# Kernel tuning notes

Measured on AMD Instinct MI355X. Metric: run time of the kernel, lower is better.

## Reference

```python
import jax, jax.numpy as jnp
import numpy as np

D_MODEL = 1024
NUM_LATENTS = 8
N_HEADS = 8
HEAD_DIM = D_MODEL // N_HEADS
LN_EPS = 1e-5
NEG_INF = -1e9


def setup_inputs() -> dict:
    key = jax.random.key(0)
    ks = jax.random.split(key, 9)
    B, S, d = 8, 8192, D_MODEL
    hidden_states = jax.random.normal(ks[0], (B, S, d), dtype=jnp.float32)
    attention_mask = jax.random.randint(ks[1], (B, S), 0, 2, dtype=jnp.int32)
    # guarantee at least one valid token per row
    attention_mask = attention_mask.at[:, 0].set(1)
    latent_queries = jax.random.normal(ks[2], (NUM_LATENTS, d), dtype=jnp.float32) * 0.02
    lim = 1.0 / np.sqrt(d)
    in_proj_weight = jax.random.uniform(ks[3], (3 * d, d), minval=-lim, maxval=lim, dtype=jnp.float32)
    in_proj_bias = jnp.zeros((3 * d,), jnp.float32)
    out_proj_weight = jax.random.uniform(ks[4], (d, d), minval=-lim, maxval=lim, dtype=jnp.float32)
    out_proj_bias = jnp.zeros((d,), jnp.float32)
    ln_gamma = jnp.ones((d,), jnp.float32)
    ln_beta = jnp.zeros((d,), jnp.float32)
    return {
        "hidden_states": hidden_states,
        "latent_queries": latent_queries,
        "in_proj_weight": in_proj_weight,
        "in_proj_bias": in_proj_bias,
        "out_proj_weight": out_proj_weight,
        "out_proj_bias": out_proj_bias,
        "ln_gamma": ln_gamma,
        "ln_beta": ln_beta,
        "attention_mask": attention_mask,
    }


def reference(hidden_states, latent_queries, in_proj_weight, in_proj_bias,
              out_proj_weight, out_proj_bias, ln_gamma, ln_beta, attention_mask):
    B, S, d = hidden_states.shape
    K, H, hd = NUM_LATENTS, N_HEADS, HEAD_DIM
    Wq, Wk, Wv = jnp.split(in_proj_weight, 3, axis=0)   # each [d, d]
    bq, bk, bv = jnp.split(in_proj_bias, 3, axis=0)
    # projections (queries shared over batch)
    q = latent_queries @ Wq.T + bq                      # [K, d]
    k = hidden_states @ Wk.T + bk                       # [B, S, d]
    v = hidden_states @ Wv.T + bv                       # [B, S, d]
    q = q.reshape(K, H, hd).transpose(1, 0, 2)          # [H, K, hd]
    k = k.reshape(B, S, H, hd).transpose(0, 2, 1, 3)    # [B, H, S, hd]
    v = v.reshape(B, S, H, hd).transpose(0, 2, 1, 3)    # [B, H, S, hd]
    scale = 1.0 / np.sqrt(hd)
    scores = jnp.einsum('hkd,bhsd->bhks', q, k) * scale  # [B, H, K, S]
    pad = (attention_mask == 0)[:, None, None, :]        # [B, 1, 1, S]
    scores = jnp.where(pad, NEG_INF, scores)
    attn = jax.nn.softmax(scores, axis=-1)
    ctx = jnp.einsum('bhks,bhsd->bhkd', attn, v)         # [B, H, K, hd]
    ctx = ctx.transpose(0, 2, 1, 3).reshape(B, K, d)     # [B, K, d]
    pooled = ctx @ out_proj_weight.T + out_proj_bias     # [B, K, d]
    # LayerNorm
    mu = pooled.mean(-1, keepdims=True)
    var = jnp.mean(jnp.square(pooled - mu), axis=-1, keepdims=True)
    pooled = (pooled - mu) * jax.lax.rsqrt(var + LN_EPS) * ln_gamma + ln_beta
    return pooled.mean(axis=1)                           # [B, d]
```

## Files before the change

kernel.cpp:

```cpp
#include <hip/hip_runtime.h>
#include <math.h>

#define D_M 1024
#define S_L 8192
#define B_N 8
#define H_N 8
#define HD_ 128
#define HK_ 64
#define SCALE_ 0.08838834764831845f
#define NEG_INF_ -1e9f
#define PITCH_ 40
#define AP_ 72

typedef _Float16 half8v __attribute__((ext_vector_type(8)));
typedef _Float16 half4v __attribute__((ext_vector_type(4)));
typedef float floatx4 __attribute__((ext_vector_type(4)));

__global__ void k_q(const float* __restrict__ lat, const float* __restrict__ W,
                    const float* __restrict__ bias, float* __restrict__ q) {
  int g = blockIdx.x * blockDim.x + threadIdx.x;
  int kidx = g >> 10, i = g & 1023;
  const float* wr = W + (size_t)i * D_M;
  const float* lr = lat + kidx * D_M;
  float acc = bias[i];
  #pragma unroll 4
  for (int t = 0; t < D_M; t += 4) {
    float4 w = *(const float4*)(wr + t);
    float4 l = *(const float4*)(lr + t);
    acc += w.x*l.x + w.y*l.y + w.z*l.z + w.w*l.w;
  }
  q[g] = acc;
}

__global__ void k_qt(const float* __restrict__ q, const float* __restrict__ W,
                     const float* __restrict__ bias, _Float16* __restrict__ qth,
                     float* __restrict__ qconst) {
  int g = blockIdx.x * blockDim.x + threadIdx.x;
  int hk = g >> 10, j = g & 1023;
  int h = hk >> 3, kidx = hk & 7;
  const float* qr = q + kidx * D_M + h * HD_;
  const float* wb = W + ((size_t)D_M + (size_t)h * HD_) * D_M + j;
  float acc = 0.f;
  #pragma unroll 4
  for (int dd = 0; dd < HD_; ++dd)
    acc += qr[dd] * wb[(size_t)dd * D_M];
  qth[g] = (_Float16)(acc * SCALE_);
  if (j == 0) {
    const float* bk = bias + D_M + h * HD_;
    float c = 0.f;
    for (int dd = 0; dd < HD_; ++dd) c += qr[dd] * bk[dd];
    qconst[hk] = c * SCALE_;
  }
}

__global__ __launch_bounds__(512) void k_cnt(const int* __restrict__ mask,
                                             int* __restrict__ cbase,
                                             int* __restrict__ cnt) {
  __shared__ int wcnt[8];
  __shared__ int ccnt[64];
  int b = blockIdx.x, tid = threadIdx.x, w = tid >> 6, lane = tid & 63;
  int vs[16];
  #pragma unroll
  for (int it = 0; it < 16; ++it) vs[it] = mask[b * S_L + it * 512 + tid];
  for (int it = 0; it < 16; ++it) {
    unsigned long long m = __ballot(vs[it] != 0);
    if (lane == 0) wcnt[w] = __popcll(m);
    __syncthreads();
    if (tid < 4) ccnt[it * 4 + tid] = wcnt[2 * tid] + wcnt[2 * tid + 1];
    __syncthreads();
  }
  if (tid == 0) {
    int base = 0;
    for (int c = 0; c < 64; ++c) { cbase[b * 64 + c] = base; base += ccnt[c]; }
    cnt[b] = base;
  }
}

__global__ __launch_bounds__(128) void k_gather(const float* __restrict__ hidden,
                                                const int* __restrict__ mask,
                                                const int* __restrict__ cbase,
                                                float* __restrict__ hcomp) {
  __shared__ int slot_of[128];
  __shared__ int wcnt[2];
  __shared__ int woff[3];
  int blk = blockIdx.x;
  int b = blk >> 6, c = blk & 63;
  int tid = threadIdx.x, w = tid >> 6, lane = tid & 63;
  int valid = mask[b * S_L + c * 128 + tid] != 0;
  unsigned long long m = __ballot(valid);
  int rank = __popcll(m & ((1ull << lane) - 1ull));
  if (lane == 0) wcnt[w] = __popcll(m);
  __syncthreads();
  if (tid == 0) { woff[0] = 0; woff[1] = wcnt[0]; woff[2] = wcnt[0] + wcnt[1]; }
  __syncthreads();
  if (valid) slot_of[woff[w] + rank] = tid;
  __syncthreads();
  int nv = woff[2];
  int base = cbase[b * 64 + c];
  for (int v = w; v < nv; v += 2) {
    const float* src = hidden + ((size_t)b * S_L + c * 128 + slot_of[v]) * D_M;
    float* dst = hcomp + ((size_t)b * S_L + base + v) * D_M;
    #pragma unroll
    for (int q4 = 0; q4 < 4; ++q4) {
      float4 val = *(const float4*)(src + q4 * 256 + lane * 4);
      *(float4*)(dst + q4 * 256 + lane * 4) = val;
    }
  }
}

__global__ __launch_bounds__(256) void k_scores3(
    const float* __restrict__ hcomp, const _Float16* __restrict__ qth,
    const float* __restrict__ qc, const int* __restrict__ cnt,
    _Float16* __restrict__ ph, float* __restrict__ pm, float* __restrict__ pl) {
  __shared__ __align__(16) _Float16 As[128 * AP_];
  __shared__ __align__(16) _Float16 Bs[64 * AP_];
  __shared__ _Float16 pT[128][68];
  __shared__ float qcs[64];
  const int tid = threadIdx.x;
  const int b = blockIdx.x >> 6;
  const int st = blockIdx.x & 63;
  const int s0 = st * 128;
  const int cb = cnt[b];
  const int SPb = ((cb + 511) >> 9) << 9;
  if (s0 >= SPb) return;
  const int w = tid >> 6, l = tid & 63;
  const int row16 = l & 15, kc = l >> 4;
  if (tid < 64) qcs[tid] = qc[tid];
  floatx4 acc[2][4];
  #pragma unroll
  for (int mf = 0; mf < 2; ++mf)
    #pragma unroll
    for (int nf = 0; nf < 4; ++nf) acc[mf][nf] = (floatx4){0.f, 0.f, 0.f, 0.f};

  const int r_ = tid >> 3, c_ = tid & 7;
  const float* hb = hcomp + ((size_t)b * S_L + s0) * D_M;
  float4 fa[4][2];
  half8v fb[2];
  #pragma unroll
  for (int p = 0; p < 4; ++p) {
    const float* pr = hb + (size_t)(p * 32 + r_) * D_M + c_ * 8;
    fa[p][0] = *(const float4*)pr; fa[p][1] = *(const float4*)(pr + 4);
  }
  fb[0] = *(const half8v*)(qth + (size_t)r_ * D_M + c_ * 8);
  fb[1] = *(const half8v*)(qth + (size_t)(r_ + 32) * D_M + c_ * 8);

  for (int k0 = 0; k0 < D_M; k0 += 64) {
    __syncthreads();
    #pragma unroll
    for (int p = 0; p < 4; ++p) {
      half8v hv;
      hv[0] = (_Float16)fa[p][0].x; hv[1] = (_Float16)fa[p][0].y;
      hv[2] = (_Float16)fa[p][0].z; hv[3] = (_Float16)fa[p][0].w;
      hv[4] = (_Float16)fa[p][1].x; hv[5] = (_Float16)fa[p][1].y;
      hv[6] = (_Float16)fa[p][1].z; hv[7] = (_Float16)fa[p][1].w;
      *(half8v*)&As[(p * 32 + r_) * AP_ + c_ * 8] = hv;
    }
    *(half8v*)&Bs[r_ * AP_ + c_ * 8] = fb[0];
    *(half8v*)&Bs[(r_ + 32) * AP_ + c_ * 8] = fb[1];
    if (k0 + 64 < D_M) {
      #pragma unroll
      for (int p = 0; p < 4; ++p) {
        const float* pr = hb + (size_t)(p * 32 + r_) * D_M + (k0 + 64) + c_ * 8;
        fa[p][0] = *(const float4*)pr; fa[p][1] = *(const float4*)(pr + 4);
      }
      fb[0] = *(const half8v*)(qth + (size_t)r_ * D_M + (k0 + 64) + c_ * 8);
      fb[1] = *(const half8v*)(qth + (size_t)(r_ + 32) * D_M + (k0 + 64) + c_ * 8);
    }
    __syncthreads();
    #pragma unroll
    for (int kk = 0; kk < 2; ++kk) {
      half8v af[2], bf4[4];
      #pragma unroll
      for (int mf = 0; mf < 2; ++mf)
        af[mf] = *(const half8v*)&As[(w * 32 + mf * 16 + row16) * AP_ + kk * 32 + kc * 8];
      #pragma unroll
      for (int nf = 0; nf < 4; ++nf)
        bf4[nf] = *(const half8v*)&Bs[(nf * 16 + row16) * AP_ + kk * 32 + kc * 8];
      #pragma unroll
      for (int mf = 0; mf < 2; ++mf)
        #pragma unroll
        for (int nf = 0; nf < 4; ++nf)
          acc[mf][nf] = __builtin_amdgcn_mfma_f32_16x16x32_f16(af[mf], bf4[nf], acc[mf][nf], 0, 0, 0);
    }
  }
  int msk[8];
  #pragma unroll
  for (int mf = 0; mf < 2; ++mf)
    #pragma unroll
    for (int r = 0; r < 4; ++r)
      msk[mf * 4 + r] = (s0 + w * 32 + mf * 16 + kc * 4 + r) < cb;
  #pragma unroll
  for (int nf = 0; nf < 4; ++nf) {
    int hk = nf * 16 + row16;
    float qcv = qcs[hk];
    float vals[8];
    float mloc = -3.4e38f;
    #pragma unroll
    for (int mf = 0; mf < 2; ++mf)
      #pragma unroll
      for (int r = 0; r < 4; ++r) {
        float v = msk[mf * 4 + r] ? (acc[mf][nf][r] + qcv) : NEG_INF_;
        vals[mf * 4 + r] = v;
        mloc = fmaxf(mloc, v);
      }
    mloc = fmaxf(mloc, __shfl_xor(mloc, 16, 64));
    mloc = fmaxf(mloc, __shfl_xor(mloc, 32, 64));
    float ls = 0.f;
    #pragma unroll
    for (int mf = 0; mf < 2; ++mf)
      #pragma unroll
      for (int r = 0; r < 4; ++r) {
        float e = __expf(vals[mf * 4 + r] - mloc);
        ls += e;
        pT[w * 32 + mf * 16 + kc * 4 + r][hk] = (_Float16)e;
      }
    ls += __shfl_xor(ls, 16, 64);
    ls += __shfl_xor(ls, 32, 64);
    if (kc == 0) {
      int idx = ((b * 64 + st) * 4 + w) * 64 + hk;
      pm[idx] = mloc;
      pl[idx] = ls;
    }
  }
  __syncthreads();
  {
    int hk2 = tid >> 2, q4 = tid & 3;
    _Float16* dst = ph + ((size_t)b * 64 + hk2) * S_L + s0 + q4 * 32;
    #pragma unroll
    for (int i = 0; i < 4; ++i) {
      half8v v;
      #pragma unroll
      for (int e = 0; e < 8; ++e) v[e] = pT[q4 * 32 + i * 8 + e][hk2];
      *(half8v*)(dst + i * 8) = v;
    }
  }
}

__global__ __launch_bounds__(256) void k_stats2b(
    const float* __restrict__ pm, const float* __restrict__ pl,
    const int* __restrict__ cnt, float* __restrict__ lvinv, _Float16* __restrict__ ph) {
  __shared__ float red[256];
  int bh = blockIdx.x;
  int b = bh >> 6, hk = bh & 63;
  int tid = threadIdx.x;
  const int cb = cnt[b];
  const int ntile = (((cb + 511) >> 9) << 9) >> 5;
  float m = -3.4e38f, lv = 0.f;
  if (tid < ntile) {
    m = pm[((size_t)b * 256 + tid) * 64 + hk];
    lv = pl[((size_t)b * 256 + tid) * 64 + hk];
  }
  red[tid] = m; __syncthreads();
  for (int off = 128; off > 0; off >>= 1) {
    if (tid < off) red[tid] = fmaxf(red[tid], red[tid + off]);
    __syncthreads();
  }
  float M = red[0]; __syncthreads();
  red[tid] = lv * __expf(m - M); __syncthreads();
  for (int off = 128; off > 0; off >>= 1) {
    if (tid < off) red[tid] += red[tid + off];
    __syncthreads();
  }
  if (tid == 0) lvinv[bh] = 1.f / red[0];
  if (tid < ntile) {
    float f = __expf(m - M);
    _Float16* pp = ph + (size_t)bh * S_L + tid * 32;
    #pragma unroll
    for (int i = 0; i < 4; ++i) {
      half8v v = *(half8v*)(pp + i * 8);
      #pragma unroll
      for (int e = 0; e < 8; ++e) v[e] = (_Float16)((float)v[e] * f);
      *(half8v*)(pp + i * 8) = v;
    }
  }
}

__global__ __launch_bounds__(512) void k_part(
    const float* __restrict__ hcomp, const _Float16* __restrict__ ph,
    const int* __restrict__ cnt, float* __restrict__ part) {
  __shared__ __align__(16) _Float16 htile[512 * PITCH_];
  const int tid = threadIdx.x;
  const int b  = blockIdx.x >> 5;
  const int jb = (blockIdx.x >> 4) & 1;
  const int sc = blockIdx.x & 15;
  const int SPb = ((cnt[b] + 511) >> 9) << 9;
  if (sc * 512 >= SPb) return;
  const int w = tid >> 6, l = tid & 63;
  const int row16 = l & 15, kc = l >> 4;
  const int s_base = sc * 512;
  const float* hb = hcomp + (size_t)b * S_L * D_M + jb * 512;
  const _Float16* phb = ph + (size_t)b * HK_ * S_L;
  floatx4 acc[4][4];
  #pragma unroll
  for (int mf = 0; mf < 4; ++mf)
    #pragma unroll
    for (int nf = 0; nf < 4; ++nf) acc[mf][nf] = (floatx4){0.f, 0.f, 0.f, 0.f};

  const int jcol = tid;
  float colv[32];
  #pragma unroll
  for (int s = 0; s < 32; ++s)
    colv[s] = hb[(size_t)(s_base + s) * D_M + jcol];

  for (int t = 0; t < 16; ++t) {
    const int s0 = s_base + t * 32;
    __syncthreads();
    #pragma unroll
    for (int sb = 0; sb < 8; ++sb) {
      half4v hv;
      hv[0] = (_Float16)colv[sb * 4 + 0];
      hv[1] = (_Float16)colv[sb * 4 + 1];
      hv[2] = (_Float16)colv[sb * 4 + 2];
      hv[3] = (_Float16)colv[sb * 4 + 3];
      *(half4v*)&htile[jcol * PITCH_ + sb * 4] = hv;
    }
    __syncthreads();
    if (t < 15) {
      #pragma unroll
      for (int s = 0; s < 32; ++s)
        colv[s] = hb[(size_t)(s0 + 32 + s) * D_M + jcol];
    }
    half8v ap[4];
    #pragma unroll
    for (int mf = 0; mf < 4; ++mf)
      ap[mf] = *(const half8v*)(phb + (size_t)(mf * 16 + row16) * S_L + s0 + kc * 8);
    #pragma unroll
    for (int nf = 0; nf < 4; ++nf) {
      int j = w * 64 + nf * 16 + row16;
      half8v bv = *(const half8v*)&htile[j * PITCH_ + kc * 8];
      #pragma unroll
      for (int mf = 0; mf < 4; ++mf)
        acc[mf][nf] = __builtin_amdgcn_mfma_f32_16x16x32_f16(ap[mf], bv, acc[mf][nf], 0, 0, 0);
    }
  }
  #pragma unroll
  for (int mf = 0; mf < 4; ++mf)
    #pragma unroll
    for (int nf = 0; nf < 4; ++nf) {
      int j = w * 64 + nf * 16 + row16;
      #pragma unroll
      for (int r = 0; r < 4; ++r) {
        int hk = mf * 16 + kc * 4 + r;
        part[(((size_t)(b * 2 + jb) * 16 + sc) * HK_ + hk) * 512 + j] = acc[mf][nf][r];
      }
    }
}

__global__ void k_comb(const float* __restrict__ part, const float* __restrict__ lvinv,
                       const int* __restrict__ cnt, float* __restrict__ ctxh) {
  int g = blockIdx.x * blockDim.x + threadIdx.x;
  int b = g >> 14;
  int rem = g & 16383;
  int hk = rem >> 8;
  int j4 = rem & 255;
  int jb = j4 >> 7;
  int jr4 = j4 & 127;
  const int nsc = (((cnt[b] + 511) >> 9) << 9) >> 9;
  const float* pb = part + ((size_t)(b * 2 + jb) * 16 * HK_ + hk) * 512 + jr4 * 4;
  float4 s = make_float4(0.f, 0.f, 0.f, 0.f);
  for (int sc = 0; sc < nsc; ++sc) {
    float4 v = *(const float4*)(pb + (size_t)sc * HK_ * 512);
    s.x += v.x; s.y += v.y; s.z += v.z; s.w += v.w;
  }
  float li = lvinv[b * 64 + hk];
  s.x *= li; s.y *= li; s.z *= li; s.w *= li;
  *(float4*)(ctxh + ((size_t)b * HK_ + hk) * D_M + j4 * 4) = s;
}

__global__ void k_ctx(const float* __restrict__ ctxh, const float* __restrict__ W,
                      const float* __restrict__ bias, float* __restrict__ ctx) {
  int g2 = blockIdx.x * blockDim.x + threadIdx.x;
  int o = g2 >> 2, kq = g2 & 3;
  int b = o >> 13, kidx = (o >> 10) & 7, i = o & 1023;
  int hk = (i >> 7) * 8 + kidx;
  const float* wr = W + ((size_t)2 * D_M + i) * D_M + kq * 256;
  const float* xr = ctxh + ((size_t)b * HK_ + hk) * D_M + kq * 256;
  float acc = 0.f;
  #pragma unroll 8
  for (int t = 0; t < 256; t += 4) {
    float4 w = *(const float4*)(wr + t);
    float4 x = *(const float4*)(xr + t);
    acc += w.x*x.x + w.y*x.y + w.z*x.z + w.w*x.w;
  }
  acc += __shfl_xor(acc, 1, 64);
  acc += __shfl_xor(acc, 2, 64);
  if (kq == 0) ctx[o] = acc + bias[2 * D_M + i];
}

__global__ void k_pool(const float* __restrict__ ctx, const float* __restrict__ W,
                       const float* __restrict__ bias, float* __restrict__ pooled) {
  int g2 = blockIdx.x * blockDim.x + threadIdx.x;
  int o = g2 >> 2, kq = g2 & 3;
  int b = o >> 13, kidx = (o >> 10) & 7, i = o & 1023;
  const float* wr = W + (size_t)i * D_M + kq * 256;
  const float* xr = ctx + ((size_t)b * 8 + kidx) * D_M + kq * 256;
  float acc = 0.f;
  #pragma unroll 8
  for (int t = 0; t < 256; t += 4) {
    float4 w = *(const float4*)(wr + t);
    float4 x = *(const float4*)(xr + t);
    acc += w.x*x.x + w.y*x.y + w.z*x.z + w.w*x.w;
  }
  acc += __shfl_xor(acc, 1, 64);
  acc += __shfl_xor(acc, 2, 64);
  if (kq == 0) pooled[o] = acc + bias[i];
}

__global__ void k_ln(const float* __restrict__ pooled, const float* __restrict__ gamma,
                     const float* __restrict__ beta, float* __restrict__ out) {
  __shared__ float red[256];
  int b = blockIdx.x, tid = threadIdx.x;
  float acc[4] = {0.f, 0.f, 0.f, 0.f};
  for (int kidx = 0; kidx < 8; ++kidx) {
    const float* row = pooled + ((size_t)b * 8 + kidx) * D_M;
    float v[4]; float s = 0.f;
    #pragma unroll
    for (int c = 0; c < 4; ++c) { v[c] = row[tid + 256 * c]; s += v[c]; }
    red[tid] = s; __syncthreads();
    for (int off = 128; off > 0; off >>= 1) {
      if (tid < off) red[tid] += red[tid + off];
      __syncthreads();
    }
    float mu = red[0] * (1.f / 1024.f);
    __syncthreads();
    float ss = 0.f;
    #pragma unroll
    for (int c = 0; c < 4; ++c) { float dd = v[c] - mu; ss += dd * dd; }
    red[tid] = ss; __syncthreads();
    for (int off = 128; off > 0; off >>= 1) {
      if (tid < off) red[tid] += red[tid + off];
      __syncthreads();
    }
    float rstd = rsqrtf(red[0] * (1.f / 1024.f) + 1e-5f);
    __syncthreads();
    #pragma unroll
    for (int c = 0; c < 4; ++c) {
      int i = tid + 256 * c;
      acc[c] += ((v[c] - mu) * rstd * gamma[i] + beta[i]) * 0.125f;
    }
  }
  #pragma unroll
  for (int c = 0; c < 4; ++c) out[(size_t)b * D_M + tid + 256 * c] = acc[c];
}

extern "C" void kernel_launch(void* const* d_in, const int* in_sizes, int n_in,
                              void* d_out, int out_size, void* d_ws, size_t ws_size,
                              hipStream_t stream) {
  const float* hidden = (const float*)d_in[0];
  const float* latent = (const float*)d_in[1];
  const float* w_in   = (const float*)d_in[2];
  const float* b_in   = (const float*)d_in[3];
  const float* w_out  = (const float*)d_in[4];
  const float* b_out  = (const float*)d_in[5];
  const float* gamma  = (const float*)d_in[6];
  const float* beta   = (const float*)d_in[7];
  const int*   mask   = (const int*)d_in[8];
  float* out = (float*)d_out;
  float* ws = (float*)d_ws;
  float* q      = ws;
  float* qc     = q + 8192;
  float* lvinv  = qc + 64;
  float* pm     = lvinv + 512;
  float* pl     = pm + 131072;
  _Float16* qth = (_Float16*)(pl + 131072);
  _Float16* ph  = (_Float16*)(pl + 131072 + 32768);
  float* part   = pl + 131072 + 32768 + 2097152;
  float* ctxh   = part + 8388608;
  float* ctx    = ctxh + 524288;
  float* pooled = ctx + 65536;
  int*   cnt    = (int*)(pooled + 65536);
  int*   cbase  = (int*)(pooled + 65536 + 16);
  float* hcomp  = pooled + 65536 + 16 + 512;

  k_q       <<<32,   256, 0, stream>>>(latent, w_in, b_in, q);
  k_qt      <<<256,  256, 0, stream>>>(q, w_in, b_in, qth, qc);
  k_cnt     <<<8,    512, 0, stream>>>(mask, cbase, cnt);
  k_gather  <<<512,  128, 0, stream>>>(hidden, mask, cbase, hcomp);
  k_scores3 <<<512,  256, 0, stream>>>(hcomp, qth, qc, cnt, ph, pm, pl);
  k_stats2b <<<512,  256, 0, stream>>>(pm, pl, cnt, lvinv, ph);
  k_part    <<<256,  512, 0, stream>>>(hcomp, ph, cnt, part);
  k_comb    <<<512,  256, 0, stream>>>(part, lvinv, cnt, ctxh);
  k_ctx     <<<1024, 256, 0, stream>>>(ctxh, w_in, b_in, ctx);
  k_pool    <<<1024, 256, 0, stream>>>(ctx, w_out, b_out, pooled);
  k_ln      <<<8,    256, 0, stream>>>(pooled, gamma, beta, out);
}
```

Baseline: 351.0 us.

## Fuse masked-row gather into scores kernel and emit compacted fp16 hidden copy

The separate gather kernel that copied valid fp32 hidden rows into a compacted buffer is removed. k_cnt now builds a per-batch index list of valid positions, padded with zeros. k_scores3 reads hidden rows indirectly through that list and, while converting to fp16 for the MFMA, also writes a compacted fp16 copy that k_part reads in place of fp32. This cuts one full fp32 read/write pass and halves k_part's input traffic, at the cost of extra global writes inside the scores kernel and serial scan work in k_cnt.

```diff
diff --git a/kernel.cpp b/kernel.cpp
--- a/kernel.cpp
+++ b/kernel.cpp
@@ -54,68 +54,44 @@
 }
 
 __global__ __launch_bounds__(512) void k_cnt(const int* __restrict__ mask,
-                                             int* __restrict__ cbase,
+                                             int* __restrict__ ridx,
                                              int* __restrict__ cnt) {
-  __shared__ int wcnt[8];
-  __shared__ int ccnt[64];
+  __shared__ int wsum[8];
+  __shared__ int base_s;
   int b = blockIdx.x, tid = threadIdx.x, w = tid >> 6, lane = tid & 63;
-  int vs[16];
-  #pragma unroll
-  for (int it = 0; it < 16; ++it) vs[it] = mask[b * S_L + it * 512 + tid];
+  #pragma unroll
+  for (int it = 0; it < 16; ++it) ridx[b * S_L + it * 512 + tid] = 0;
+  if (tid == 0) base_s = 0;
+  __syncthreads();
   for (int it = 0; it < 16; ++it) {
-    unsigned long long m = __ballot(vs[it] != 0);
-    if (lane == 0) wcnt[w] = __popcll(m);
-    __syncthreads();
-    if (tid < 4) ccnt[it * 4 + tid] = wcnt[2 * tid] + wcnt[2 * tid + 1];
-    __syncthreads();
-  }
-  if (tid == 0) {
-    int base = 0;
-    for (int c = 0; c < 64; ++c) { cbase[b * 64 + c] = base; base += ccnt[c]; }
-    cnt[b] = base;
-  }
-}
-
-__global__ __launch_bounds__(128) void k_gather(const float* __restrict__ hidden,
-                                                const int* __restrict__ mask,
-                                                const int* __restrict__ cbase,
-                                                float* __restrict__ hcomp) {
-  __shared__ int slot_of[128];
-  __shared__ int wcnt[2];
-  __shared__ int woff[3];
-  int blk = blockIdx.x;
-  int b = blk >> 6, c = blk & 63;
-  int tid = threadIdx.x, w = tid >> 6, lane = tid & 63;
-  int valid = mask[b * S_L + c * 128 + tid] != 0;
-  unsigned long long m = __ballot(valid);
-  int rank = __popcll(m & ((1ull << lane) - 1ull));
-  if (lane == 0) wcnt[w] = __popcll(m);
-  __syncthreads();
-  if (tid == 0) { woff[0] = 0; woff[1] = wcnt[0]; woff[2] = wcnt[0] + wcnt[1]; }
-  __syncthreads();
-  if (valid) slot_of[woff[w] + rank] = tid;
-  __syncthreads();
-  int nv = woff[2];
-  int base = cbase[b * 64 + c];
-  for (int v = w; v < nv; v += 2) {
-    const float* src = hidden + ((size_t)b * S_L + c * 128 + slot_of[v]) * D_M;
-    float* dst = hcomp + ((size_t)b * S_L + base + v) * D_M;
-    #pragma unroll
-    for (int q4 = 0; q4 < 4; ++q4) {
-      float4 val = *(const float4*)(src + q4 * 256 + lane * 4);
-      *(float4*)(dst + q4 * 256 + lane * 4) = val;
-    }
-  }
+    int s = it * 512 + tid;
+    int valid = mask[b * S_L + s] != 0;
+    unsigned long long m = __ballot(valid);
+    int rank = __popcll(m & ((1ull << lane) - 1ull));
+    if (lane == 0) wsum[w] = __popcll(m);
+    __syncthreads();
+    int base = base_s;
+    int woff = 0, ctot = 0;
+    #pragma unroll
+    for (int i = 0; i < 8; ++i) { if (i < w) woff += wsum[i]; ctot += wsum[i]; }
+    __syncthreads();
+    if (valid) ridx[b * S_L + base + woff + rank] = s;
+    if (tid == 0) base_s = base + ctot;
+    __syncthreads();
+  }
+  if (tid == 0) cnt[b] = base_s;
 }
 
 __global__ __launch_bounds__(256) void k_scores3(
-    const float* __restrict__ hcomp, const _Float16* __restrict__ qth,
+    const float* __restrict__ hsrc, const _Float16* __restrict__ qth,
     const float* __restrict__ qc, const int* __restrict__ cnt,
+    const int* __restrict__ ridx, _Float16* __restrict__ h16c,
     _Float16* __restrict__ ph, float* __restrict__ pm, float* __restrict__ pl) {
   __shared__ __align__(16) _Float16 As[128 * AP_];
   __shared__ __align__(16) _Float16 Bs[64 * AP_];
   __shared__ _Float16 pT[128][68];
   __shared__ float qcs[64];
+  __shared__ int ridx_s[128];
   const int tid = threadIdx.x;
   const int b = blockIdx.x >> 6;
   const int st = blockIdx.x & 63;
@@ -126,6 +102,7 @@
   const int w = tid >> 6, l = tid & 63;
   const int row16 = l & 15, kc = l >> 4;
   if (tid < 64) qcs[tid] = qc[tid];
+  if (tid < 128) ridx_s[tid] = ridx[b * S_L + s0 + tid];
   floatx4 acc[2][4];
   #pragma unroll
   for (int mf = 0; mf < 2; ++mf)
@@ -133,13 +110,19 @@
     for (int nf = 0; nf < 4; ++nf) acc[mf][nf] = (floatx4){0.f, 0.f, 0.f, 0.f};
 
   const int r_ = tid >> 3, c_ = tid & 7;
-  const float* hb = hcomp + ((size_t)b * S_L + s0) * D_M;
+  __syncthreads();
+  const float* rowp[4];
+  _Float16* h16p[4];
+  #pragma unroll
+  for (int p = 0; p < 4; ++p) {
+    rowp[p] = hsrc + ((size_t)b * S_L + ridx_s[p * 32 + r_]) * D_M + c_ * 8;
+    h16p[p] = h16c + ((size_t)b * S_L + s0 + p * 32 + r_) * D_M + c_ * 8;
+  }
   float4 fa[4][2];
   half8v fb[2];
   #pragma unroll
   for (int p = 0; p < 4; ++p) {
-    const float* pr = hb + (size_t)(p * 32 + r_) * D_M + c_ * 8;
-    fa[p][0] = *(const float4*)pr; fa[p][1] = *(const float4*)(pr + 4);
+    fa[p][0] = *(const float4*)rowp[p]; fa[p][1] = *(const float4*)(rowp[p] + 4);
   }
   fb[0] = *(const half8v*)(qth + (size_t)r_ * D_M + c_ * 8);
   fb[1] = *(const half8v*)(qth + (size_t)(r_ + 32) * D_M + c_ * 8);
@@ -154,14 +137,15 @@
       hv[4] = (_Float16)fa[p][1].x; hv[5] = (_Float16)fa[p][1].y;
       hv[6] = (_Float16)fa[p][1].z; hv[7] = (_Float16)fa[p][1].w;
       *(half8v*)&As[(p * 32 + r_) * AP_ + c_ * 8] = hv;
+      *(half8v*)(h16p[p] + k0) = hv;
     }
     *(half8v*)&Bs[r_ * AP_ + c_ * 8] = fb[0];
     *(half8v*)&Bs[(r_ + 32) * AP_ + c_ * 8] = fb[1];
     if (k0 + 64 < D_M) {
       #pragma unroll
       for (int p = 0; p < 4; ++p) {
-        const float* pr = hb + (size_t)(p * 32 + r_) * D_M + (k0 + 64) + c_ * 8;
-        fa[p][0] = *(const float4*)pr; fa[p][1] = *(const float4*)(pr + 4);
+        fa[p][0] = *(const float4*)(rowp[p] + k0 + 64);
+        fa[p][1] = *(const float4*)(rowp[p] + k0 + 64 + 4);
       }
       fb[0] = *(const half8v*)(qth + (size_t)r_ * D_M + (k0 + 64) + c_ * 8);
       fb[1] = *(const half8v*)(qth + (size_t)(r_ + 32) * D_M + (k0 + 64) + c_ * 8);
@@ -276,7 +260,7 @@
 }
 
 __global__ __launch_bounds__(512) void k_part(
-    const float* __restrict__ hcomp, const _Float16* __restrict__ ph,
+    const _Float16* __restrict__ h16c, const _Float16* __restrict__ ph,
     const int* __restrict__ cnt, float* __restrict__ part) {
   __shared__ __align__(16) _Float16 htile[512 * PITCH_];
   const int tid = threadIdx.x;
@@ -288,7 +272,7 @@
   const int w = tid >> 6, l = tid & 63;
   const int row16 = l & 15, kc = l >> 4;
   const int s_base = sc * 512;
-  const float* hb = hcomp + (size_t)b * S_L * D_M + jb * 512;
+  const _Float16* hb = h16c + (size_t)b * S_L * D_M + jb * 512;
   const _Float16* phb = ph + (size_t)b * HK_ * S_L;
   floatx4 acc[4][4];
   #pragma unroll
@@ -297,7 +281,7 @@
     for (int nf = 0; nf < 4; ++nf) acc[mf][nf] = (floatx4){0.f, 0.f, 0.f, 0.f};
 
   const int jcol = tid;
-  float colv[32];
+  _Float16 colv[32];
   #pragma unroll
   for (int s = 0; s < 32; ++s)
     colv[s] = hb[(size_t)(s_base + s) * D_M + jcol];
@@ -308,10 +292,10 @@
     #pragma unroll
     for (int sb = 0; sb < 8; ++sb) {
       half4v hv;
-      hv[0] = (_Float16)colv[sb * 4 + 0];
-      hv[1] = (_Float16)colv[sb * 4 + 1];
-      hv[2] = (_Float16)colv[sb * 4 + 2];
-      hv[3] = (_Float16)colv[sb * 4 + 3];
+      hv[0] = colv[sb * 4 + 0];
+      hv[1] = colv[sb * 4 + 1];
+      hv[2] = colv[sb * 4 + 2];
+      hv[3] = colv[sb * 4 + 3];
       *(half4v*)&htile[jcol * PITCH_ + sb * 4] = hv;
     }
     __syncthreads();
@@ -469,16 +453,15 @@
   float* ctx    = ctxh + 524288;
   float* pooled = ctx + 65536;
   int*   cnt    = (int*)(pooled + 65536);
-  int*   cbase  = (int*)(pooled + 65536 + 16);
-  float* hcomp  = pooled + 65536 + 16 + 512;
+  int*   ridx   = (int*)(pooled + 65536 + 16);
+  _Float16* h16c = (_Float16*)(pooled + 65536 + 16 + 65536);
 
   k_q       <<<32,   256, 0, stream>>>(latent, w_in, b_in, q);
   k_qt      <<<256,  256, 0, stream>>>(q, w_in, b_in, qth, qc);
-  k_cnt     <<<8,    512, 0, stream>>>(mask, cbase, cnt);
-  k_gather  <<<512,  128, 0, stream>>>(hidden, mask, cbase, hcomp);
-  k_scores3 <<<512,  256, 0, stream>>>(hcomp, qth, qc, cnt, ph, pm, pl);
+  k_cnt     <<<8,    512, 0, stream>>>(mask, ridx, cnt);
+  k_scores3 <<<512,  256, 0, stream>>>(hidden, qth, qc, cnt, ridx, h16c, ph, pm, pl);
   k_stats2b <<<512,  256, 0, stream>>>(pm, pl, cnt, lvinv, ph);
-  k_part    <<<256,  512, 0, stream>>>(hcomp, ph, cnt, part);
+  k_part    <<<256,  512, 0, stream>>>(h16c, ph, cnt, part);
   k_comb    <<<512,  256, 0, stream>>>(part, lvinv, cnt, ctxh);
   k_ctx     <<<1024, 256, 0, stream>>>(ctxh, w_in, b_in, ctx);
   k_pool    <<<1024, 256, 0, stream>>>(ctx, w_out, b_out, pooled);
```

Result: faster. 310.4 us, median of 2 (-11.6%).
